# Kernel tuning notes

Hardware: AMD Instinct MI355X
Metric: run time of the kernel (lower is better)

The kernel has to match this reference:

```python
import jax, jax.numpy as jnp
import numpy as np

D = 1024
H = 16
HD = D // H  # 64


def setup_inputs() -> dict:
    key = jax.random.key(0)
    ks = jax.random.split(key, 10)
    s = 0.02
    return {
        "x": jax.random.normal(ks[0], (2, 2048, D), dtype=jnp.float32),
        "rel_bias": jax.random.normal(ks[1], (H, 2048, 2048), dtype=jnp.float32),
        "Wq": jax.random.normal(ks[2], (D, D), dtype=jnp.float32) * s,
        "bq": jnp.zeros((D,), dtype=jnp.float32),
        "Wk": jax.random.normal(ks[3], (D, D), dtype=jnp.float32) * s,
        "bk": jnp.zeros((D,), dtype=jnp.float32),
        "Wv": jax.random.normal(ks[4], (D, D), dtype=jnp.float32) * s,
        "bv": jnp.zeros((D,), dtype=jnp.float32),
        "Wo": jax.random.normal(ks[5], (D, D), dtype=jnp.float32) * s,
        "bo": jnp.zeros((D,), dtype=jnp.float32),
    }


def reference(x, rel_bias, Wq, bq, Wk, bk, Wv, bv, Wo, bo):
    B, L, _ = x.shape
    # QKV projections -> [B, H, L, HD]
    def proj(W, b):
        return (x @ W.T + b).reshape(B, L, H, HD).transpose(0, 2, 1, 3)
    q = proj(Wq, bq)
    k = proj(Wk, bk)
    v = proj(Wv, bv)
    scale = 1.0 / jnp.sqrt(jnp.float32(HD))
    scores = jnp.einsum("bhqd,bhkd->bhqk", q, k) * scale + rel_bias[None]
    attn = jax.nn.softmax(scores, axis=-1)  # dropout p=0 -> identity
    out = jnp.einsum("bhqk,bhkd->bhqd", attn, v)
    out = out.transpose(0, 2, 1, 3).reshape(B, L, H * HD)
    return out @ Wo.T + bo
```

## Files before the change

kernel.cpp:

```cpp
#include <hip/hip_runtime.h>


typedef __attribute__((ext_vector_type(8))) short bf16x8;
typedef __attribute__((ext_vector_type(4))) float f32x4;
typedef __attribute__((ext_vector_type(16))) float f32x16;
typedef __attribute__((ext_vector_type(8))) unsigned short u16x8;
using u16 = unsigned short;

#define MFMA16(a, b, c) __builtin_amdgcn_mfma_f32_16x16x32_bf16((a), (b), (c), 0, 0, 0)
#define MFMA32(a, b, c) __builtin_amdgcn_mfma_f32_32x32x16_bf16((a), (b), (c), 0, 0, 0)
#define LOG2E 1.44269504088896f
#define QSCALE (0.125f * 1.44269504088896f)

__device__ __forceinline__ u16 f2bf(float f) {
  union { float f; unsigned int u; } v; v.f = f;
  unsigned int r = v.u + 0x7FFFu + ((v.u >> 16) & 1u);
  return (u16)(r >> 16);
}

__device__ __forceinline__ unsigned cvt_pk_bf16(float lo, float hi) {
  unsigned r;
  asm volatile("v_cvt_pk_bf16_f32 %0, %1, %2" : "=v"(r) : "v"(lo), "v"(hi));
  return r;
}

__device__ __forceinline__ void pl32swap(unsigned& a, unsigned& b) {
#if __has_builtin(__builtin_amdgcn_permlane32_swap)
  typedef unsigned pl2 __attribute__((ext_vector_type(2)));
  pl2 r = __builtin_amdgcn_permlane32_swap(a, b, false, false);
  a = r[0];
  b = r[1];
#else
  asm volatile("v_permlane32_swap_b32 %0, %1" : "+v"(a), "+v"(b));
#endif
}

__device__ __forceinline__ void g2lds16(const void* gsrc, void* ldst) {
  __builtin_amdgcn_global_load_lds(
      (const __attribute__((address_space(1))) unsigned int*)gsrc,
      (__attribute__((address_space(3))) unsigned int*)ldst, 16, 0, 0);
}

__global__ __launch_bounds__(256) void cvt_all(
    const float* __restrict__ x, const float* __restrict__ wq,
    const float* __restrict__ wk, const float* __restrict__ wv,
    const float* __restrict__ wo, u16* __restrict__ xb,
    u16* __restrict__ w1b, u16* __restrict__ wob) {
  int bid = blockIdx.x, tid = threadIdx.x;
  const float* src; u16* dst; int i;
  if (bid < 2048)      { src = x;  dst = xb;            i = bid * 256 + tid; }
  else if (bid < 2560) { src = wq; dst = w1b;           i = (bid - 2048) * 256 + tid; }
  else if (bid < 3072) { src = wk; dst = w1b + (1<<20); i = (bid - 2560) * 256 + tid; }
  else if (bid < 3584) { src = wv; dst = w1b + (2<<20); i = (bid - 3072) * 256 + tid; }
  else                 { src = wo; dst = wob;           i = (bid - 3584) * 256 + tid; }
  const float4* s = (const float4*)src;
  float4 a = s[2 * i], b = s[2 * i + 1];
  u16x8 o;
  o[0] = f2bf(a.x); o[1] = f2bf(a.y); o[2] = f2bf(a.z); o[3] = f2bf(a.w);
  o[4] = f2bf(b.x); o[5] = f2bf(b.y); o[6] = f2bf(b.z); o[7] = f2bf(b.w);
  ((u16x8*)dst)[i] = o;
}

template <int MODE>
__global__ __launch_bounds__(256, 2) void gemm_bt(
    const u16* __restrict__ A, const u16* __restrict__ B,
    u16* __restrict__ qp, u16* __restrict__ kp, u16* __restrict__ vp,
    const float* __restrict__ b0, const float* __restrict__ b1,
    const float* __restrict__ b2, float* __restrict__ outp,
    const float* __restrict__ bo) {
  __shared__ __align__(16) u16 lA[128 * 64];
  __shared__ __align__(16) u16 lB[128 * 64];
  const int tid = threadIdx.x;
  const int lane = tid & 63, wid = tid >> 6;
  const int g = lane >> 4, cc = lane & 15;
  const int wr = wid >> 1, wc = wid & 1;
  const int m0 = blockIdx.y * 128, n0 = blockIdx.x * 128;
  f32x4 acc[4][4] = {};
  for (int kt = 0; kt < 16; ++kt) {
    const int kof = kt * 64;
#pragma unroll
    for (int i = 0; i < 4; ++i) {
      int cid = i * 256 + tid;
      int row = cid >> 3;
      int col = (cid & 7) * 8;
      g2lds16(A + (size_t)(m0 + row) * 1024 + kof + col, &lA[(i * 256 + wid * 64) * 8]);
      g2lds16(B + (size_t)(n0 + row) * 1024 + kof + col, &lB[(i * 256 + wid * 64) * 8]);
    }
    __syncthreads();
#pragma unroll
    for (int kc = 0; kc < 2; ++kc) {
      bf16x8 af[4], bfr[4];
#pragma unroll
      for (int mf = 0; mf < 4; ++mf)
        af[mf] = *(const bf16x8*)&lA[(wr * 64 + mf * 16 + cc) * 64 + kc * 32 + g * 8];
#pragma unroll
      for (int nf = 0; nf < 4; ++nf)
        bfr[nf] = *(const bf16x8*)&lB[(wc * 64 + nf * 16 + cc) * 64 + kc * 32 + g * 8];
#pragma unroll
      for (int mf = 0; mf < 4; ++mf)
#pragma unroll
        for (int nf = 0; nf < 4; ++nf)
          acc[mf][nf] = MFMA16(af[mf], bfr[nf], acc[mf][nf]);
    }
    __syncthreads();
  }
#pragma unroll
  for (int mf = 0; mf < 4; ++mf) {
#pragma unroll
    for (int nf = 0; nf < 4; ++nf) {
      int n = n0 + wc * 64 + nf * 16 + cc;
      if (MODE == 0) {
        int which = n >> 10;
        int nn = n & 1023;
        const float* bp = which == 0 ? b0 : (which == 1 ? b1 : b2);
        float bias = bp[nn];
        int h = nn >> 6, hd = nn & 63;
        int mb = m0 + wr * 64 + mf * 16 + g * 4;
        int bb = mb >> 11, ll0 = mb & 2047;
        if (which == 2) {
          ushort4 pk4;
          pk4.x = f2bf(acc[mf][nf][0] + bias);
          pk4.y = f2bf(acc[mf][nf][1] + bias);
          pk4.z = f2bf(acc[mf][nf][2] + bias);
          pk4.w = f2bf(acc[mf][nf][3] + bias);
          *(ushort4*)&vp[(((size_t)(bb * 16 + h)) * 64 + hd) * 2048 + ll0] = pk4;
        } else {
          u16* dp = which == 0 ? qp : kp;
#pragma unroll
          for (int r = 0; r < 4; ++r) {
            float val = acc[mf][nf][r] + bias;
            if (which == 0) val *= QSCALE;
            dp[(((size_t)(bb * 16 + h)) * 2048 + ll0 + r) * 64 + hd] = f2bf(val);
          }
        }
      } else {
        float bias = bo[n];
#pragma unroll
        for (int r = 0; r < 4; ++r) {
          int m = m0 + wr * 64 + mf * 16 + g * 4 + r;
          outp[(size_t)m * 1024 + n] = acc[mf][nf][r] + bias;
        }
      }
    }
  }
}

__global__ __launch_bounds__(512, 1) void attn_kernel(
    const u16* __restrict__ qm, const u16* __restrict__ km,
    const u16* __restrict__ vtm, const float* __restrict__ bias,
    u16* __restrict__ aout) {
  __shared__ __align__(16) unsigned char smem[98304];
  const int tid = threadIdx.x;
  const int lane = tid & 63, wid = tid >> 6;
  const int lq = lane & 31, hi = lane >> 5;
  const int s = wid & 3, b = wid >> 2;
  const int lin = blockIdx.x;
  const int xcd = lin & 7, j = lin >> 3;
  const int h = xcd * 2 + (j >> 4);
  const int qb = j & 15;
  const int q0 = qb * 128;
  const u16* kg0 = km + ((size_t)0 * 16 + h) * 2048 * 64;
  const u16* kg1 = km + ((size_t)1 * 16 + h) * 2048 * 64;
  const u16* vg0 = vtm + ((size_t)0 * 16 + h) * 64 * 2048;
  const u16* vg1 = vtm + ((size_t)1 * 16 + h) * 64 * 2048;
  const float* bg = bias + (size_t)h * 2048 * 2048;
  const size_t bh = (size_t)b * 16 + h;
  const u16* qbase = qm + (bh * 2048 + q0 + s * 32) * 64;

  bf16x8 qf[4];
#pragma unroll
  for (int i = 0; i < 4; ++i)
    qf[i] = *(const bf16x8*)&qbase[(size_t)lq * 64 + i * 16 + 8 * hi];

  f32x16 o[2];
#pragma unroll
  for (int r = 0; r < 16; ++r) { o[0][r] = 0.f; o[1][r] = 0.f; }
  float lsum = 0.f;

#define STAGE_P(BI, k0n)                                                       \
  {                                                                            \
    unsigned char* base = smem + (BI) * 32768;                                 \
    unsigned char* kdst = base + 16384;                                        \
    unsigned char* vdst = base + 24576;                                        \
    _Pragma("unroll") for (int i = 0; i < 2; ++i) {                            \
      int slot = i * 512 + tid;                                                \
      int row = slot >> 3, ch = slot & 7;                                      \
      g2lds16(bg + (size_t)(q0 + row) * 2048 + (k0n) + ((ch ^ (row & 7)) << 2),\
              base + slot * 16);                                               \
    }                                                                          \
    {                                                                          \
      int bb = tid >> 8, kr = (tid >> 3) & 31, ch = tid & 7;                   \
      const u16* kgp = bb ? kg1 : kg0;                                         \
      g2lds16(kgp + (size_t)((k0n) + kr) * 64 + ((ch ^ (kr & 7)) << 3),        \
              kdst + tid * 16);                                                \
    }                                                                          \
    {                                                                          \
      int bb = tid >> 8, d = (tid >> 2) & 63, ch = tid & 3;                    \
      const u16* vgp = bb ? vg1 : vg0;                                         \
      g2lds16(vgp + (size_t)d * 2048 + (k0n) + ((ch ^ (d & 3)) << 3),          \
              vdst + tid * 16);                                                \
    }                                                                          \
  }

  STAGE_P(0, 0)
  STAGE_P(1, 32)
  __builtin_amdgcn_sched_barrier(0);

#pragma unroll 1
  for (int p = 0; p < 64; ++p) {
    const int BI = p % 3;
    if (p < 63) { asm volatile("s_waitcnt vmcnt(4)" ::: "memory"); }
    else        { asm volatile("s_waitcnt vmcnt(0)" ::: "memory"); }
    __builtin_amdgcn_sched_barrier(0);
    __builtin_amdgcn_s_barrier();
    __builtin_amdgcn_sched_barrier(0);
    if (p + 2 < 64) { STAGE_P((p + 2) % 3, (p + 2) * 32) }
    __builtin_amdgcn_sched_barrier(0);
    const u16* lKp = (const u16*)(smem + BI * 32768 + 16384 + b * 4096);
    const u16* lVp = (const u16*)(smem + BI * 32768 + 24576 + b * 4096);
    const float4* lB = (const float4*)(smem + BI * 32768);
    f32x16 acc;
#pragma unroll
    for (int r = 0; r < 16; ++r) acc[r] = -32.0f;
#pragma unroll
    for (int i = 0; i < 4; ++i) {
      bf16x8 kf = *(const bf16x8*)&lKp[lq * 64 + (((2 * i + hi) ^ (lq & 7))) * 8];
      acc = MFMA32(kf, qf[i], acc);
    }
    const int brow = s * 32 + lq;
#pragma unroll
    for (int g = 0; g < 4; ++g) {
      float4 b4 = lB[brow * 8 + ((2 * g + hi) ^ (brow & 7))];
      acc[g * 4 + 0] = fmaf(b4.x, LOG2E, acc[g * 4 + 0]);
      acc[g * 4 + 1] = fmaf(b4.y, LOG2E, acc[g * 4 + 1]);
      acc[g * 4 + 2] = fmaf(b4.z, LOG2E, acc[g * 4 + 2]);
      acc[g * 4 + 3] = fmaf(b4.w, LOG2E, acc[g * 4 + 3]);
    }
#pragma unroll
    for (int r = 0; r < 16; ++r) {
      acc[r] = __builtin_amdgcn_exp2f(acc[r]);
      lsum += acc[r];
    }
    unsigned c0 = cvt_pk_bf16(acc[0], acc[1]),   c1 = cvt_pk_bf16(acc[2], acc[3]);
    unsigned c2 = cvt_pk_bf16(acc[4], acc[5]),   c3 = cvt_pk_bf16(acc[6], acc[7]);
    unsigned c4 = cvt_pk_bf16(acc[8], acc[9]),   c5 = cvt_pk_bf16(acc[10], acc[11]);
    unsigned c6 = cvt_pk_bf16(acc[12], acc[13]), c7 = cvt_pk_bf16(acc[14], acc[15]);
    pl32swap(c0, c2); pl32swap(c1, c3);
    pl32swap(c4, c6); pl32swap(c5, c7);
    union { unsigned u[4]; bf16x8 v; } a0, a1;
    a0.u[0] = c0; a0.u[1] = c1; a0.u[2] = c2; a0.u[3] = c3;
    a1.u[0] = c4; a1.u[1] = c5; a1.u[2] = c6; a1.u[3] = c7;
#pragma unroll
    for (int dblk = 0; dblk < 2; ++dblk) {
      int rowv = dblk * 32 + lq;
      bf16x8 v0 = *(const bf16x8*)&lVp[rowv * 32 + ((hi ^ (rowv & 3))) * 8];
      bf16x8 v1 = *(const bf16x8*)&lVp[rowv * 32 + (((2 + hi) ^ (rowv & 3))) * 8];
      o[dblk] = MFMA32(a0.v, v0, o[dblk]);
      o[dblk] = MFMA32(a1.v, v1, o[dblk]);
    }
    __builtin_amdgcn_sched_barrier(0);
  }
#undef STAGE_P

  lsum += __shfl_xor(lsum, 32, 64);
  float linv = 1.0f / lsum;
#pragma unroll
  for (int r = 0; r < 16; ++r) {
    int qr = (r & 3) + 8 * (r >> 2) + 4 * hi;
    float lr = __shfl(linv, qr, 64);
    size_t base = ((size_t)b * 2048 + q0 + s * 32 + qr) * 1024 + h * 64 + lq;
    aout[base] = f2bf(o[0][r] * lr);
    aout[base + 32] = f2bf(o[1][r] * lr);
  }
}

extern "C" void kernel_launch(void* const* d_in, const int* in_sizes, int n_in,
                              void* d_out, int out_size, void* d_ws, size_t ws_size,
                              hipStream_t stream) {
  const float* x  = (const float*)d_in[0];
  const float* rb = (const float*)d_in[1];
  const float* Wq = (const float*)d_in[2];
  const float* bq = (const float*)d_in[3];
  const float* Wk = (const float*)d_in[4];
  const float* bk = (const float*)d_in[5];
  const float* Wv = (const float*)d_in[6];
  const float* bv = (const float*)d_in[7];
  const float* Wo = (const float*)d_in[8];
  const float* bo = (const float*)d_in[9];
  float* out = (float*)d_out;
  char* ws = (char*)d_ws;

  u16* xb   = (u16*)(ws);
  u16* W1b  = (u16*)(ws + (8 << 20));
  u16* Wob  = (u16*)(ws + (14 << 20));
  u16* qb   = (u16*)(ws + (16 << 20));
  u16* kb2  = (u16*)(ws + (24 << 20));
  u16* vtb  = (u16*)(ws + (32 << 20));
  u16* aout = xb;

  cvt_all<<<4096, 256, 0, stream>>>(x, Wq, Wk, Wv, Wo, xb, W1b, Wob);
  gemm_bt<0><<<dim3(24, 32), 256, 0, stream>>>(xb, W1b, qb, kb2, vtb, bq, bk, bv,
                                               nullptr, nullptr);
  attn_kernel<<<256, 512, 0, stream>>>(qb, kb2, vtb, rb, aout);
  gemm_bt<1><<<dim3(8, 32), 256, 0, stream>>>(aout, Wob, nullptr, nullptr, nullptr,
                                              nullptr, nullptr, nullptr, out, bo);
}
```

Measured before the change: 176.0 us.

## Replace triple-buffered direct-to-LDS loads with register-staged double buffering at two blocks per CU

The attention kernel previously streamed bias, K and V tiles with direct global-to-LDS loads into three 32 KB LDS buffers. It now loads each tile into registers one iteration ahead, writes them into one of two LDS buffers after compute, and synchronises. The LDS footprint falls from 96 KB to 64 KB and launch bounds request two blocks per CU, aiming for more occupancy to hide latency. In exchange it adds register pressure, extra LDS write instructions and a full vmcnt(0) wait each iteration, so prefetch depth shrinks.

```diff
diff --git a/kernel.cpp b/kernel.cpp
--- a/kernel.cpp
+++ b/kernel.cpp
@@ -145,11 +145,11 @@
   }
 }
 
-__global__ __launch_bounds__(512, 1) void attn_kernel(
+__global__ __launch_bounds__(512, 2) void attn_kernel(
     const u16* __restrict__ qm, const u16* __restrict__ km,
     const u16* __restrict__ vtm, const float* __restrict__ bias,
     u16* __restrict__ aout) {
-  __shared__ __align__(16) unsigned char smem[98304];
+  __shared__ __align__(16) unsigned char smem[65536];
   const int tid = threadIdx.x;
   const int lane = tid & 63, wid = tid >> 6;
   const int lq = lane & 31, hi = lane >> 5;
@@ -159,14 +159,24 @@
   const int h = xcd * 2 + (j >> 4);
   const int qb = j & 15;
   const int q0 = qb * 128;
-  const u16* kg0 = km + ((size_t)0 * 16 + h) * 2048 * 64;
-  const u16* kg1 = km + ((size_t)1 * 16 + h) * 2048 * 64;
-  const u16* vg0 = vtm + ((size_t)0 * 16 + h) * 64 * 2048;
-  const u16* vg1 = vtm + ((size_t)1 * 16 + h) * 64 * 2048;
   const float* bg = bias + (size_t)h * 2048 * 2048;
   const size_t bh = (size_t)b * 16 + h;
   const u16* qbase = qm + (bh * 2048 + q0 + s * 32) * 64;
 
+  const int brow_a = tid >> 3, bch = tid & 7;
+  const float* bsrcA = bg + (size_t)(q0 + brow_a) * 2048 + ((bch ^ (brow_a & 7)) << 2);
+  const float* bsrcB = bg + (size_t)(q0 + 64 + brow_a) * 2048 + ((bch ^ ((64 + brow_a) & 7)) << 2);
+  {
+  }
+  const int kbb = tid >> 8, kr = (tid >> 3) & 31, kch = tid & 7;
+  const u16* ksrc = km + ((size_t)kbb * 16 + h) * 2048 * 64 + (size_t)kr * 64 +
+                    ((kch ^ (kr & 7)) << 3);
+  const int vbb = tid >> 8, vd = (tid >> 2) & 63, vch = tid & 3;
+  const u16* vsrc = vtm + ((size_t)vbb * 16 + h) * 64 * 2048 + (size_t)vd * 2048 +
+                    ((vch ^ (vd & 3)) << 3);
+  const int dA = tid * 16, dB = (512 + tid) * 16;
+  const int dK = 16384 + tid * 16, dV = 24576 + tid * 16;
+
   bf16x8 qf[4];
 #pragma unroll
   for (int i = 0; i < 4; ++i)
@@ -177,90 +187,95 @@
   for (int r = 0; r < 16; ++r) { o[0][r] = 0.f; o[1][r] = 0.f; }
   float lsum = 0.f;
 
-#define STAGE_P(BI, k0n)                                                       \
+  float4 rA, rB, rK, rV;
+
+#define ISSUE_LOADS()                                                          \
   {                                                                            \
-    unsigned char* base = smem + (BI) * 32768;                                 \
-    unsigned char* kdst = base + 16384;                                        \
-    unsigned char* vdst = base + 24576;                                        \
-    _Pragma("unroll") for (int i = 0; i < 2; ++i) {                            \
-      int slot = i * 512 + tid;                                                \
-      int row = slot >> 3, ch = slot & 7;                                      \
-      g2lds16(bg + (size_t)(q0 + row) * 2048 + (k0n) + ((ch ^ (row & 7)) << 2),\
-              base + slot * 16);                                               \
-    }                                                                          \
-    {                                                                          \
-      int bb = tid >> 8, kr = (tid >> 3) & 31, ch = tid & 7;                   \
-      const u16* kgp = bb ? kg1 : kg0;                                         \
-      g2lds16(kgp + (size_t)((k0n) + kr) * 64 + ((ch ^ (kr & 7)) << 3),        \
-              kdst + tid * 16);                                                \
-    }                                                                          \
-    {                                                                          \
-      int bb = tid >> 8, d = (tid >> 2) & 63, ch = tid & 3;                    \
-      const u16* vgp = bb ? vg1 : vg0;                                         \
-      g2lds16(vgp + (size_t)d * 2048 + (k0n) + ((ch ^ (d & 3)) << 3),          \
-              vdst + tid * 16);                                                \
-    }                                                                          \
-  }
-
-  STAGE_P(0, 0)
-  STAGE_P(1, 32)
+    rA = *(const float4*)bsrcA;                                                \
+    rB = *(const float4*)bsrcB;                                                \
+    rK = *(const float4*)ksrc;                                                 \
+    rV = *(const float4*)vsrc;                                                 \
+    bsrcA += 32; bsrcB += 32; ksrc += 32 * 64; vsrc += 32;                     \
+  }
+
+#define WRITE_LDS(BI)                                                          \
+  {                                                                            \
+    unsigned char* base_ = smem + (BI) * 32768;                                \
+    *(float4*)(base_ + dA) = rA;                                               \
+    *(float4*)(base_ + dB) = rB;                                               \
+    *(float4*)(base_ + dK) = rK;                                               \
+    *(float4*)(base_ + dV) = rV;                                               \
+  }
+
+  ISSUE_LOADS()
   __builtin_amdgcn_sched_barrier(0);
+  asm volatile("s_waitcnt vmcnt(0)" ::: "memory");
+  __builtin_amdgcn_sched_barrier(0);
+  WRITE_LDS(0)
+  ISSUE_LOADS()
+  __builtin_amdgcn_sched_barrier(0);
+  __syncthreads();
 
 #pragma unroll 1
   for (int p = 0; p < 64; ++p) {
-    const int BI = p % 3;
-    if (p < 63) { asm volatile("s_waitcnt vmcnt(4)" ::: "memory"); }
-    else        { asm volatile("s_waitcnt vmcnt(0)" ::: "memory"); }
-    __builtin_amdgcn_sched_barrier(0);
-    __builtin_amdgcn_s_barrier();
-    __builtin_amdgcn_sched_barrier(0);
-    if (p + 2 < 64) { STAGE_P((p + 2) % 3, (p + 2) * 32) }
-    __builtin_amdgcn_sched_barrier(0);
-    const u16* lKp = (const u16*)(smem + BI * 32768 + 16384 + b * 4096);
-    const u16* lVp = (const u16*)(smem + BI * 32768 + 24576 + b * 4096);
-    const float4* lB = (const float4*)(smem + BI * 32768);
-    f32x16 acc;
-#pragma unroll
-    for (int r = 0; r < 16; ++r) acc[r] = -32.0f;
-#pragma unroll
-    for (int i = 0; i < 4; ++i) {
-      bf16x8 kf = *(const bf16x8*)&lKp[lq * 64 + (((2 * i + hi) ^ (lq & 7))) * 8];
-      acc = MFMA32(kf, qf[i], acc);
-    }
-    const int brow = s * 32 + lq;
-#pragma unroll
-    for (int g = 0; g < 4; ++g) {
-      float4 b4 = lB[brow * 8 + ((2 * g + hi) ^ (brow & 7))];
-      acc[g * 4 + 0] = fmaf(b4.x, LOG2E, acc[g * 4 + 0]);
-      acc[g * 4 + 1] = fmaf(b4.y, LOG2E, acc[g * 4 + 1]);
-      acc[g * 4 + 2] = fmaf(b4.z, LOG2E, acc[g * 4 + 2]);
-      acc[g * 4 + 3] = fmaf(b4.w, LOG2E, acc[g * 4 + 3]);
-    }
-#pragma unroll
-    for (int r = 0; r < 16; ++r) {
-      acc[r] = __builtin_amdgcn_exp2f(acc[r]);
-      lsum += acc[r];
-    }
-    unsigned c0 = cvt_pk_bf16(acc[0], acc[1]),   c1 = cvt_pk_bf16(acc[2], acc[3]);
-    unsigned c2 = cvt_pk_bf16(acc[4], acc[5]),   c3 = cvt_pk_bf16(acc[6], acc[7]);
-    unsigned c4 = cvt_pk_bf16(acc[8], acc[9]),   c5 = cvt_pk_bf16(acc[10], acc[11]);
-    unsigned c6 = cvt_pk_bf16(acc[12], acc[13]), c7 = cvt_pk_bf16(acc[14], acc[15]);
-    pl32swap(c0, c2); pl32swap(c1, c3);
-    pl32swap(c4, c6); pl32swap(c5, c7);
-    union { unsigned u[4]; bf16x8 v; } a0, a1;
-    a0.u[0] = c0; a0.u[1] = c1; a0.u[2] = c2; a0.u[3] = c3;
-    a1.u[0] = c4; a1.u[1] = c5; a1.u[2] = c6; a1.u[3] = c7;
-#pragma unroll
-    for (int dblk = 0; dblk < 2; ++dblk) {
-      int rowv = dblk * 32 + lq;
-      bf16x8 v0 = *(const bf16x8*)&lVp[rowv * 32 + ((hi ^ (rowv & 3))) * 8];
-      bf16x8 v1 = *(const bf16x8*)&lVp[rowv * 32 + (((2 + hi) ^ (rowv & 3))) * 8];
-      o[dblk] = MFMA32(a0.v, v0, o[dblk]);
-      o[dblk] = MFMA32(a1.v, v1, o[dblk]);
-    }
-    __builtin_amdgcn_sched_barrier(0);
-  }
-#undef STAGE_P
+    const int BI = p & 1;
+    {
+      const u16* lKp = (const u16*)(smem + BI * 32768 + 16384 + b * 4096);
+      const u16* lVp = (const u16*)(smem + BI * 32768 + 24576 + b * 4096);
+      const float4* lB = (const float4*)(smem + BI * 32768);
+      f32x16 acc;
+#pragma unroll
+      for (int r = 0; r < 16; ++r) acc[r] = -32.0f;
+#pragma unroll
+      for (int i = 0; i < 4; ++i) {
+        bf16x8 kf = *(const bf16x8*)&lKp[lq * 64 + (((2 * i + hi) ^ (lq & 7))) * 8];
+        acc = MFMA32(kf, qf[i], acc);
+      }
+      const int brow = s * 32 + lq;
+#pragma unroll
+      for (int g = 0; g < 4; ++g) {
+        float4 b4 = lB[brow * 8 + ((2 * g + hi) ^ (brow & 7))];
+        acc[g * 4 + 0] = fmaf(b4.x, LOG2E, acc[g * 4 + 0]);
+        acc[g * 4 + 1] = fmaf(b4.y, LOG2E, acc[g * 4 + 1]);
+        acc[g * 4 + 2] = fmaf(b4.z, LOG2E, acc[g * 4 + 2]);
+        acc[g * 4 + 3] = fmaf(b4.w, LOG2E, acc[g * 4 + 3]);
+      }
+#pragma unroll
+      for (int r = 0; r < 16; ++r) {
+        acc[r] = __builtin_amdgcn_exp2f(acc[r]);
+        lsum += acc[r];
+      }
+      unsigned c0 = cvt_pk_bf16(acc[0], acc[1]),   c1 = cvt_pk_bf16(acc[2], acc[3]);
+      unsigned c2 = cvt_pk_bf16(acc[4], acc[5]),   c3 = cvt_pk_bf16(acc[6], acc[7]);
+      unsigned c4 = cvt_pk_bf16(acc[8], acc[9]),   c5 = cvt_pk_bf16(acc[10], acc[11]);
+      unsigned c6 = cvt_pk_bf16(acc[12], acc[13]), c7 = cvt_pk_bf16(acc[14], acc[15]);
+      pl32swap(c0, c2); pl32swap(c1, c3);
+      pl32swap(c4, c6); pl32swap(c5, c7);
+      union { unsigned u[4]; bf16x8 v; } a0, a1;
+      a0.u[0] = c0; a0.u[1] = c1; a0.u[2] = c2; a0.u[3] = c3;
+      a1.u[0] = c4; a1.u[1] = c5; a1.u[2] = c6; a1.u[3] = c7;
+#pragma unroll
+      for (int dblk = 0; dblk < 2; ++dblk) {
+        int rowv = dblk * 32 + lq;
+        bf16x8 v0 = *(const bf16x8*)&lVp[rowv * 32 + ((hi ^ (rowv & 3))) * 8];
+        bf16x8 v1 = *(const bf16x8*)&lVp[rowv * 32 + (((2 + hi) ^ (rowv & 3))) * 8];
+        o[dblk] = MFMA32(a0.v, v0, o[dblk]);
+        o[dblk] = MFMA32(a1.v, v1, o[dblk]);
+      }
+    }
+    if (p < 63) {
+      __builtin_amdgcn_sched_barrier(0);
+      asm volatile("s_waitcnt vmcnt(0)" ::: "memory");
+      __builtin_amdgcn_sched_barrier(0);
+      WRITE_LDS(BI ^ 1)
+      __builtin_amdgcn_sched_barrier(0);
+      if (p < 62) { ISSUE_LOADS() }
+      __builtin_amdgcn_sched_barrier(0);
+      __syncthreads();
+    }
+  }
+#undef WRITE_LDS
+#undef ISSUE_LOADS
 
   lsum += __shfl_xor(lsum, 32, 64);
   float linv = 1.0f / lsum;
```

New measurement: 157.6 us. 10.5% less time.
